# Kernel optimization log

Hardware: AMD Instinct MI355X
Metric: run time of the kernel (lower is better)

The kernel has to match this reference:

```python
import jax, jax.numpy as jnp
import numpy as np

N = 10000   # nodes
E = 100000  # edges (before self-loops)
H = 4       # heads (layers 0-3); last layer uses 1 head
C = 200     # out_channels per head
IN_DIMS = [200, H * C, H * C, H * C, H * C]
HEADS   = [H, H, H, H, 1]
NEG_SLOPE = 0.2  # PyG GATConv default


def _gat_layer(x, src, dst, W, a_src, a_dst, b, heads):
    # x: [N, Fin], W: [Fin, heads*C], a_src/a_dst: [heads, C], b: [heads*C]
    h = (x @ W).reshape(N, heads, C)                       # [N,H,C]
    alpha_src = jnp.einsum('nhc,hc->nh', h, a_src)         # [N,H]
    alpha_dst = jnp.einsum('nhc,hc->nh', h, a_dst)         # [N,H]
    e = jax.nn.leaky_relu(alpha_src[src] + alpha_dst[dst], NEG_SLOPE)  # [E',H]
    # segment softmax over incoming edges of each dst node
    m = jax.ops.segment_max(e, dst, num_segments=N)        # [N,H]
    ex = jnp.exp(e - m[dst])                               # [E',H]
    den = jax.ops.segment_sum(ex, dst, num_segments=N)     # [N,H]
    alpha = ex / den[dst]                                  # [E',H]
    out = jax.ops.segment_sum(h[src] * alpha[:, :, None], dst, num_segments=N)
    return out.reshape(N, heads * C) + b, alpha


def setup_inputs() -> dict:
    key = jax.random.key(0)
    ks = jax.random.split(key, 2 + 4 * 5)
    inp = {}
    inp['X'] = jax.random.normal(ks[0], (N, 200), jnp.float32)
    inp['edge_index'] = jax.random.randint(ks[1], (2, E), 0, N, dtype=jnp.int32)
    k = 2
    for i in range(5):
        fin, hd = IN_DIMS[i], HEADS[i]
        s = 1.0 / np.sqrt(fin)
        inp[f'W{i}'] = jax.random.normal(ks[k], (fin, hd * C), jnp.float32) * s; k += 1
        inp[f'as{i}'] = jax.random.normal(ks[k], (hd, C), jnp.float32) * s; k += 1
        inp[f'ad{i}'] = jax.random.normal(ks[k], (hd, C), jnp.float32) * s; k += 1
        inp[f'b{i}'] = jnp.zeros((hd * C,), jnp.float32); k += 1
    return inp


def reference(X, edge_index,
              W0, as0, ad0, b0, W1, as1, ad1, b1, W2, as2, ad2, b2,
              W3, as3, ad3, b3, W4, as4, ad4, b4):
    # add self-loops (PyG GATConv default add_self_loops=True)
    loops = jnp.arange(N, dtype=edge_index.dtype)
    src = jnp.concatenate([edge_index[0], loops])
    dst = jnp.concatenate([edge_index[1], loops])
    gelu = lambda v: jax.nn.gelu(v, approximate=False)
    # eval mode: all dropouts are identity
    x, _ = _gat_layer(X, src, dst, W0, as0, ad0, b0, HEADS[0]); x = gelu(x)
    x, _ = _gat_layer(x, src, dst, W1, as1, ad1, b1, HEADS[1]); x = gelu(x)
    x, _ = _gat_layer(x, src, dst, W2, as2, ad2, b2, HEADS[2]); x = gelu(x)
    x, _ = _gat_layer(x, src, dst, W3, as3, ad3, b3, HEADS[3]); x = gelu(x)
    x, edge_attn = _gat_layer(x, src, dst, W4, as4, ad4, b4, HEADS[4])
    x = gelu(x)
    return (x, edge_attn)
```

## Files before the change

### kernel.cpp

```cpp
#include <hip/hip_runtime.h>
#include <math.h>

#define NN 10000
#define EE 100000
#define EPE 110000
#define CC 200
#define MPAD 10112

typedef __attribute__((ext_vector_type(8))) _Float16 f16x8;
typedef __attribute__((ext_vector_type(4))) _Float16 f16x4;
typedef __attribute__((ext_vector_type(4))) unsigned short u16x4;
typedef __attribute__((ext_vector_type(4))) float f32x4;

__device__ __forceinline__ float lrelu(float v) { return v >= 0.f ? v : 0.2f * v; }
__device__ __forceinline__ float gelu_f(float v) { return 0.5f * v * (1.f + erff(v * 0.70710678118654752f)); }


__global__ void build_edges_kernel(const int* __restrict__ ei,
                                   int* __restrict__ src_all, int* __restrict__ dst_all,
                                   int* __restrict__ deg) {
    int e = blockIdx.x * blockDim.x + threadIdx.x;
    if (e >= EPE) return;
    int s, d;
    if (e < EE) { s = ei[e]; d = ei[EE + e]; }
    else        { s = e - EE; d = e - EE; }
    src_all[e] = s;
    dst_all[e] = d;
    atomicAdd(&deg[d], 1);
}

__global__ void scan_kernel(const int* __restrict__ deg, int* __restrict__ row_ptr, int n) {
    __shared__ int wsum[16];
    int tid = threadIdx.x;
    int lane = tid & 63, w = tid >> 6;
    int carry = 0;
    for (int base = 0; base < n; base += 1024) {
        int idx = base + tid;
        int v = (idx < n) ? deg[idx] : 0;
        int x = v;
#pragma unroll
        for (int off = 1; off < 64; off <<= 1) {
            int t = __shfl_up(x, off);
            if (lane >= off) x += t;
        }
        if (lane == 63) wsum[w] = x;
        __syncthreads();
        if (w == 0) {
            int s = (lane < 16) ? wsum[lane] : 0;
#pragma unroll
            for (int off = 1; off < 16; off <<= 1) {
                int t = __shfl_up(s, off);
                if (lane >= off) s += t;
            }
            if (lane < 16) wsum[lane] = s;
        }
        __syncthreads();
        int woff = (w > 0) ? wsum[w - 1] : 0;
        if (idx < n) row_ptr[idx] = carry + woff + x - v;
        carry += wsum[15];
        __syncthreads();
    }
    if (tid == 0) row_ptr[n] = carry;
}

__global__ void scatter_kernel(const int* __restrict__ src_all, const int* __restrict__ dst_all,
                               const int* __restrict__ row_ptr, int* __restrict__ cursor,
                               int* __restrict__ col_src, int* __restrict__ col_eid) {
    int e = blockIdx.x * blockDim.x + threadIdx.x;
    if (e >= EPE) return;
    int d = dst_all[e];
    int pos = row_ptr[d] + atomicAdd(&cursor[d], 1);
    col_src[pos] = src_all[e];
    col_eid[pos] = e;
}


__global__ void convA_kernel(const float* __restrict__ x, int sx, int Fin, int Kp,
                             unsigned short* __restrict__ Ap) {
    size_t idx = (size_t)blockIdx.x * 256 + threadIdx.x;
    if (idx >= (size_t)MPAD * Kp) return;
    int row = (int)(idx / Kp);
    int kk  = (int)(idx % Kp);
    float v = 0.f;
    if (row < NN && kk < Fin) v = x[(size_t)row * sx + kk];
    Ap[idx] = __builtin_bit_cast(unsigned short, (_Float16)v);
}

__global__ void padA_kernel(unsigned short* __restrict__ Ap) {
    int idx = blockIdx.x * 256 + threadIdx.x;
    if (idx < NN * 32) {
        int rw = idx >> 5, c = idx & 31;
        Ap[(size_t)rw * 832 + 800 + c] = 0;
    } else {
        int j = idx - NN * 32;
        if (j < (MPAD - NN) * 832) {
            int rw = j / 832, c = j - rw * 832;
            Ap[(size_t)(NN + rw) * 832 + c] = 0;
        }
    }
}

__global__ void convB_kernel(const float* __restrict__ W, int Fin, int HC, int Kp, int Np,
                             unsigned short* __restrict__ Bp) {
    size_t idx = (size_t)blockIdx.x * 256 + threadIdx.x;
    if (idx >= (size_t)Np * Kp) return;
    int n  = (int)(idx / Kp);
    int kk = (int)(idx % Kp);
    float v = 0.f;
    if (n < HC && kk < Fin) v = W[(size_t)kk * HC + n];
    Bp[idx] = __builtin_bit_cast(unsigned short, (_Float16)v);
}


__global__ __launch_bounds__(256) void gemm_mfma(const unsigned short* __restrict__ A,
                                                 const unsigned short* __restrict__ B,
                                                 unsigned short* __restrict__ C,
                                                 int Kt, int Np, int ncol) {
    __shared__ unsigned short As[2][4096];
    __shared__ unsigned short Bs[2][8192];

    int tid = threadIdx.x;
    int lane = tid & 63, wave = tid >> 6;

    int nwg = gridDim.x;
    int orig = blockIdx.x;
    int q = nwg >> 3, r = nwg & 7;
    int xcd = orig & 7, sidx = orig >> 3;
    int wg = (xcd < r ? xcd * (q + 1) : r * (q + 1) + (xcd - r) * q) + sidx;
    int rowT = wg / ncol, colT = wg - rowT * ncol;
    int row0 = rowT * 64, col0 = colT * 128;
    int wr = wave >> 1, wc = wave & 1;

    size_t gAoff[2], gBoff[4];
    int ldsSegA[2], ldsSegB[4];
#pragma unroll
    for (int i = 0; i < 2; ++i) {
        int seg = wave * 2 + i;
        int chunkIdx = seg * 64 + lane;
        int rr = chunkIdx >> 3;
        int c = chunkIdx & 7;
        int cg = c ^ (rr & 7);
        gAoff[i] = (size_t)(row0 + rr) * Kt + (size_t)cg * 8;
        ldsSegA[i] = seg * 512;
    }
#pragma unroll
    for (int i = 0; i < 4; ++i) {
        int seg = wave * 4 + i;
        int chunkIdx = seg * 64 + lane;
        int rr = chunkIdx >> 3;
        int c = chunkIdx & 7;
        int cg = c ^ (rr & 7);
        gBoff[i] = (size_t)(col0 + rr) * Kt + (size_t)cg * 8;
        ldsSegB[i] = seg * 512;
    }

    int rowA[2], rowB[4];
#pragma unroll
    for (int m = 0; m < 2; ++m) rowA[m] = wr * 32 + m * 16 + (lane & 15);
#pragma unroll
    for (int n = 0; n < 4; ++n) rowB[n] = wc * 64 + n * 16 + (lane & 15);

    f32x4 acc[2][4];
#pragma unroll
    for (int m = 0; m < 2; ++m)
#pragma unroll
        for (int n = 0; n < 4; ++n) acc[m][n] = f32x4{0.f, 0.f, 0.f, 0.f};

#define STAGE(bufi, kk)                                                                     \
    _Pragma("unroll")                                                                       \
    for (int i = 0; i < 2; ++i)                                                             \
        __builtin_amdgcn_global_load_lds(                                                   \
            (const __attribute__((address_space(1))) void*)(A + gAoff[i] + (kk)),           \
            (__attribute__((address_space(3))) void*)(&As[bufi][ldsSegA[i]]), 16, 0, 0);    \
    _Pragma("unroll")                                                                       \
    for (int i = 0; i < 4; ++i)                                                             \
        __builtin_amdgcn_global_load_lds(                                                   \
            (const __attribute__((address_space(1))) void*)(B + gBoff[i] + (kk)),           \
            (__attribute__((address_space(3))) void*)(&Bs[bufi][ldsSegB[i]]), 16, 0, 0);

    int nk = Kt >> 6;
    STAGE(0, 0)

    for (int t = 0; t < nk; ++t) {
        int cur = t & 1;
        if (t + 1 < nk) {
            STAGE(1 - cur, (t + 1) * 64)
            asm volatile("s_waitcnt vmcnt(6)" ::: "memory");
        } else {
            asm volatile("s_waitcnt vmcnt(0)" ::: "memory");
        }
        __builtin_amdgcn_s_barrier();
        __builtin_amdgcn_sched_barrier(0);

        const unsigned short* asb = As[cur];
        const unsigned short* bsb = Bs[cur];
#pragma unroll
        for (int kh = 0; kh < 2; ++kh) {
            int cw = kh * 4 + (lane >> 4);
            f16x8 a[2], b[4];
#pragma unroll
            for (int m = 0; m < 2; ++m) {
                int ia = rowA[m] * 64 + ((cw ^ (rowA[m] & 7)) << 3);
                a[m] = *(const f16x8*)(&asb[ia]);
            }
#pragma unroll
            for (int n = 0; n < 4; ++n) {
                int ib = rowB[n] * 64 + ((cw ^ (rowB[n] & 7)) << 3);
                b[n] = *(const f16x8*)(&bsb[ib]);
            }
            if (kh == 0) __builtin_amdgcn_s_setprio(1);
#pragma unroll
            for (int m = 0; m < 2; ++m)
#pragma unroll
                for (int n = 0; n < 4; ++n)
                    acc[m][n] = __builtin_amdgcn_mfma_f32_16x16x32_f16(a[m], b[n], acc[m][n], 0, 0, 0);
        }
        __builtin_amdgcn_s_setprio(0);
        asm volatile("s_waitcnt lgkmcnt(0)" ::: "memory");
        __builtin_amdgcn_sched_barrier(0);
        __builtin_amdgcn_s_barrier();
        __builtin_amdgcn_sched_barrier(0);
    }
#undef STAGE

    int crow = row0 + wr * 32 + ((lane >> 4) << 2);
    int ccol = col0 + wc * 64 + (lane & 15);
#pragma unroll
    for (int m = 0; m < 2; ++m)
#pragma unroll
        for (int j = 0; j < 4; ++j) {
            size_t rb = (size_t)(crow + m * 16 + j) * Np;
#pragma unroll
            for (int n = 0; n < 4; ++n)
                C[rb + ccol + n * 16] =
                    __builtin_bit_cast(unsigned short, (_Float16)acc[m][n][j]);
        }
}


__global__ void attn_kernel(const unsigned short* __restrict__ h,
                            const float* __restrict__ a_s, const float* __restrict__ a_d,
                            float* __restrict__ asrc, float* __restrict__ adst,
                            int H, int HCp) {
    int n = blockIdx.x;
    int wave = threadIdx.x >> 6;
    int lane = threadIdx.x & 63;
    if (wave >= H) return;
    float sa = 0.f, da = 0.f;
    int c0 = lane * 4;
    if (c0 < CC) {
        f16x4 hv = *(const f16x4*)(h + (size_t)n * HCp + wave * CC + c0);
        float4 av = *(const float4*)(a_s + wave * CC + c0);
        float4 dv = *(const float4*)(a_d + wave * CC + c0);
        float h0 = (float)hv[0], h1 = (float)hv[1], h2 = (float)hv[2], h3 = (float)hv[3];
        sa = h0 * av.x + h1 * av.y + h2 * av.z + h3 * av.w;
        da = h0 * dv.x + h1 * dv.y + h2 * dv.z + h3 * dv.w;
    }
#pragma unroll
    for (int off = 32; off > 0; off >>= 1) {
        sa += __shfl_down(sa, off);
        da += __shfl_down(da, off);
    }
    if (lane == 0) {
        asrc[n * H + wave] = sa;
        adst[n * H + wave] = da;
    }
}


__global__ void mden_weight_kernel(const float* __restrict__ asrc, const float* __restrict__ adst,
                                   const int* __restrict__ row_ptr, const int* __restrict__ col_src,
                                   const int* __restrict__ col_eid,
                                   float* __restrict__ w, int H) {
    int i = blockIdx.x * blockDim.x + threadIdx.x;
    if (i >= NN * H) return;
    int n = i / H, hd = i - n * H;
    float ad = adst[i];
    int beg = row_ptr[n], end = row_ptr[n + 1];
    float m = -1e30f, den = 0.f;
    for (int e = beg; e < end; ++e) {
        int s = col_src[e];
        float v = lrelu(asrc[s * H + hd] + ad);
        if (v > m) { den = den * expf(m - v) + 1.f; m = v; }
        else den += expf(v - m);
    }
    float inv = 1.f / den;
    for (int e = beg; e < end; ++e) {
        int s = col_src[e];
        float v = lrelu(asrc[s * H + hd] + ad);
        w[(size_t)col_eid[e] * H + hd] = expf(v - m) * inv;
    }
}


__global__ __launch_bounds__(256) void agg3_kernel(const unsigned short* __restrict__ h,
                                                   const float* __restrict__ w,
                                                   const int* __restrict__ row_ptr,
                                                   const int* __restrict__ col_src,
                                                   const int* __restrict__ col_eid,
                                                   const float* __restrict__ bias,
                                                   float* __restrict__ out32,
                                                   unsigned short* __restrict__ apn,
                                                   int H, int HC, int HCp) {
    int n = blockIdx.x;
    int hc0 = threadIdx.x * 4;
    if (hc0 >= HC) return;
    int head = hc0 / CC;
    int beg = row_ptr[n], end = row_ptr[n + 1];

    float a0 = 0.f, a1 = 0.f, a2 = 0.f, a3 = 0.f;
    int s = col_src[beg], eid = col_eid[beg];
    float wv = w[(size_t)eid * H + head];
    f16x4 hv = *(const f16x4*)(h + (size_t)s * HCp + hc0);
    for (int e = beg; e < end; ++e) {
        int s2 = 0, eid2 = 0; float wv2 = 0.f; f16x4 hv2 = {};
        if (e + 1 < end) {
            s2 = col_src[e + 1]; eid2 = col_eid[e + 1];
            wv2 = w[(size_t)eid2 * H + head];
            hv2 = *(const f16x4*)(h + (size_t)s2 * HCp + hc0);
        }
        a0 += wv * (float)hv[0];
        a1 += wv * (float)hv[1];
        a2 += wv * (float)hv[2];
        a3 += wv * (float)hv[3];
        s = s2; eid = eid2; wv = wv2; hv = hv2;
    }
    float4 bv = *(const float4*)(bias + hc0);
    float g0 = gelu_f(a0 + bv.x), g1 = gelu_f(a1 + bv.y);
    float g2 = gelu_f(a2 + bv.z), g3 = gelu_f(a3 + bv.w);
    if (out32) {
        *(float4*)(out32 + (size_t)n * HC + hc0) = float4{g0, g1, g2, g3};
    } else {
        *(u16x4*)(apn + (size_t)n * 832 + hc0) = u16x4{
            __builtin_bit_cast(unsigned short, (_Float16)g0),
            __builtin_bit_cast(unsigned short, (_Float16)g1),
            __builtin_bit_cast(unsigned short, (_Float16)g2),
            __builtin_bit_cast(unsigned short, (_Float16)g3)};
    }
}


extern "C" void kernel_launch(void* const* d_in, const int* in_sizes, int n_in,
                              void* d_out, int out_size, void* d_ws, size_t ws_size,
                              hipStream_t stream) {
    const float* X = (const float*)d_in[0];
    const int* ei = (const int*)d_in[1];

    char* ws = (char*)d_ws;
    size_t off = 0;
    auto alloc = [&](size_t bytes) { void* p = ws + off; off += (bytes + 255) & ~(size_t)255; return p; };

    unsigned short* Ap0 = (unsigned short*)alloc((size_t)MPAD * 256 * 2);
    unsigned short* Ap  = (unsigned short*)alloc((size_t)MPAD * 832 * 2);
    unsigned short* Bp  = (unsigned short*)alloc((size_t)896 * 832 * 2);
    unsigned short* hbuf= (unsigned short*)alloc((size_t)MPAD * 896 * 2);
    float* asrc   = (float*)alloc((size_t)NN * 4 * 4);
    float* adst   = (float*)alloc((size_t)NN * 4 * 4);
    float* wbuf   = (float*)alloc((size_t)EPE * 4 * 4);
    int* src_all  = (int*)alloc((size_t)EPE * 4);
    int* dst_all  = (int*)alloc((size_t)EPE * 4);
    int* col_src  = (int*)alloc((size_t)EPE * 4);
    int* col_eid  = (int*)alloc((size_t)EPE * 4);
    int* row_ptr  = (int*)alloc((size_t)(NN + 1) * 4);
    int* degcur   = (int*)alloc((size_t)2 * NN * 4);
    int* deg = degcur, * cursor = degcur + NN;

    hipMemsetAsync(degcur, 0, 2 * NN * sizeof(int), stream);

    int eb = (EPE + 255) / 256;
    build_edges_kernel<<<eb, 256, 0, stream>>>(ei, src_all, dst_all, deg);
    scan_kernel<<<1, 1024, 0, stream>>>(deg, row_ptr, NN);
    scatter_kernel<<<eb, 256, 0, stream>>>(src_all, dst_all, row_ptr, cursor, col_src, col_eid);

    {
        int npad = NN * 32 + (MPAD - NN) * 832;
        padA_kernel<<<(npad + 255) / 256, 256, 0, stream>>>(Ap);
    }
    {
        size_t na = (size_t)MPAD * 256;
        convA_kernel<<<(int)((na + 255) / 256), 256, 0, stream>>>(X, 200, 200, 256, Ap0);
    }

    for (int i = 0; i < 5; ++i) {
        int Fin = (i == 0) ? 200 : 800;
        int H   = (i == 4) ? 1 : 4;
        int HC  = H * CC;
        int Kp  = (Fin == 200) ? 256 : 832;
        int Np  = (HC == 800) ? 896 : 256;
        int ncol = Np / 128;
        const unsigned short* Acur = (i == 0) ? Ap0 : Ap;
        const float* W   = (const float*)d_in[2 + 4 * i];
        const float* as_ = (const float*)d_in[3 + 4 * i];
        const float* ad_ = (const float*)d_in[4 + 4 * i];
        const float* b_  = (const float*)d_in[5 + 4 * i];

        size_t nb = (size_t)Np * Kp;
        convB_kernel<<<(int)((nb + 255) / 256), 256, 0, stream>>>(W, Fin, HC, Kp, Np, Bp);

        gemm_mfma<<<ncol * (MPAD / 64), 256, 0, stream>>>(Acur, Bp, hbuf, Kp, Np, ncol);

        attn_kernel<<<NN, 256, 0, stream>>>(hbuf, as_, ad_, asrc, adst, H, Np);

        float* wptr = (i == 4) ? (float*)d_out + (size_t)NN * CC : wbuf;
        mden_weight_kernel<<<(NN * H + 255) / 256, 256, 0, stream>>>(asrc, adst, row_ptr,
                                                                     col_src, col_eid, wptr, H);

        float* out32 = (i == 4) ? (float*)d_out : nullptr;
        unsigned short* apn = (i == 4) ? nullptr : Ap;
        agg3_kernel<<<NN, 256, 0, stream>>>(hbuf, wptr, row_ptr, col_src, col_eid, b_,
                                            out32, apn, H, HC, Np);
    }
}
```

Baseline: 543.2 us.

## Fuse attention logits into GEMM epilogue and softmax into aggregation kernel

Computes the per-node source/destination attention scores inside the GEMM epilogue by reducing over each tile's accumulators and atomically adding the partial sums, which removes the separate attention kernel and its re-read of h. The segment softmax (max/denominator) moves into the aggregation kernel as a wave-parallel reduction, and edge weights are recomputed on the fly in LDS, so weights are written to global memory only for the final layer. Weight conversion for all five layers is batched into one launch. The atomics add contention and make the scores depend on summation order, and the aggregation kernel gains block-level syncs per 64-edge chunk.

```diff
diff --git a/kernel.cpp b/kernel.cpp
--- a/kernel.cpp
+++ b/kernel.cpp
@@ -100,22 +100,33 @@
     }
 }
 
-__global__ void convB_kernel(const float* __restrict__ W, int Fin, int HC, int Kp, int Np,
-                             unsigned short* __restrict__ Bp) {
-    size_t idx = (size_t)blockIdx.x * 256 + threadIdx.x;
-    if (idx >= (size_t)Np * Kp) return;
-    int n  = (int)(idx / Kp);
-    int kk = (int)(idx % Kp);
+__global__ void convB_all_kernel(const float* __restrict__ W0, const float* __restrict__ W1,
+                                 const float* __restrict__ W2, const float* __restrict__ W3,
+                                 const float* __restrict__ W4,
+                                 unsigned short* __restrict__ Bp) {
+    int l = blockIdx.y;
+    const float* W = (l == 0) ? W0 : (l == 1) ? W1 : (l == 2) ? W2 : (l == 3) ? W3 : W4;
+    int Fin = (l == 0) ? 200 : 800;
+    int HC  = (l == 4) ? 200 : 800;
+    int Kp  = (l == 0) ? 256 : 832;
+    int Np  = (l == 4) ? 256 : 896;
+    int idx = blockIdx.x * 256 + threadIdx.x;
+    if (idx >= Np * Kp) return;
+    int n = idx / Kp, kk = idx - n * Kp;
     float v = 0.f;
     if (n < HC && kk < Fin) v = W[(size_t)kk * HC + n];
-    Bp[idx] = __builtin_bit_cast(unsigned short, (_Float16)v);
+    Bp[(size_t)l * (896 * 832) + idx] = __builtin_bit_cast(unsigned short, (_Float16)v);
 }
 
 
 __global__ __launch_bounds__(256) void gemm_mfma(const unsigned short* __restrict__ A,
                                                  const unsigned short* __restrict__ B,
                                                  unsigned short* __restrict__ C,
-                                                 int Kt, int Np, int ncol) {
+                                                 const float* __restrict__ a_s,
+                                                 const float* __restrict__ a_d,
+                                                 float* __restrict__ g_asrc,
+                                                 float* __restrict__ g_adst,
+                                                 int Kt, int Np, int ncol, int HC, int H) {
     __shared__ unsigned short As[2][4096];
     __shared__ unsigned short Bs[2][8192];
 
@@ -235,107 +246,152 @@
                 C[rb + ccol + n * 16] =
                     __builtin_bit_cast(unsigned short, (_Float16)acc[m][n][j]);
         }
-}
-
-
-__global__ void attn_kernel(const unsigned short* __restrict__ h,
-                            const float* __restrict__ a_s, const float* __restrict__ a_d,
-                            float* __restrict__ asrc, float* __restrict__ adst,
-                            int H, int HCp) {
+
+    int base = col0 + wc * 64;
+    int hA = base / CC;
+    float sAs[2][8], sAd[2][8];
+#pragma unroll
+    for (int b = 0; b < 2; ++b)
+#pragma unroll
+        for (int k = 0; k < 8; ++k) { sAs[b][k] = 0.f; sAd[b][k] = 0.f; }
+#pragma unroll
+    for (int n = 0; n < 4; ++n) {
+        int c = ccol + n * 16;
+        if (c < HC) {
+            int hd = c / CC;
+            int cm = c - hd * CC;
+            float asv = a_s[hd * CC + cm];
+            float adv = a_d[hd * CC + cm];
+            int b = hd - hA;
+#pragma unroll
+            for (int m = 0; m < 2; ++m)
+#pragma unroll
+                for (int j = 0; j < 4; ++j) {
+                    sAs[b][m * 4 + j] += acc[m][n][j] * asv;
+                    sAd[b][m * 4 + j] += acc[m][n][j] * adv;
+                }
+        }
+    }
+#pragma unroll
+    for (int off = 1; off < 16; off <<= 1) {
+#pragma unroll
+        for (int b = 0; b < 2; ++b)
+#pragma unroll
+            for (int k = 0; k < 8; ++k) {
+                sAs[b][k] += __shfl_xor(sAs[b][k], off);
+                sAd[b][k] += __shfl_xor(sAd[b][k], off);
+            }
+    }
+    if ((lane & 15) == 0) {
+#pragma unroll
+        for (int b = 0; b < 2; ++b) {
+            int hd = hA + b;
+            if (hd >= H) continue;
+#pragma unroll
+            for (int m = 0; m < 2; ++m)
+#pragma unroll
+                for (int j = 0; j < 4; ++j) {
+                    int row = crow + m * 16 + j;
+                    if (row < NN) {
+                        atomicAdd(&g_asrc[row * H + hd], sAs[b][m * 4 + j]);
+                        atomicAdd(&g_adst[row * H + hd], sAd[b][m * 4 + j]);
+                    }
+                }
+        }
+    }
+}
+
+
+__global__ __launch_bounds__(256) void fused_agg_kernel(const unsigned short* __restrict__ h,
+                                                        const float* __restrict__ asrc,
+                                                        const float* __restrict__ adst,
+                                                        const int* __restrict__ row_ptr,
+                                                        const int* __restrict__ col_src,
+                                                        const int* __restrict__ col_eid,
+                                                        const float* __restrict__ bias,
+                                                        float* __restrict__ out32,
+                                                        unsigned short* __restrict__ apn,
+                                                        float* __restrict__ wout,
+                                                        int H, int HC, int HCp) {
     int n = blockIdx.x;
-    int wave = threadIdx.x >> 6;
-    int lane = threadIdx.x & 63;
-    if (wave >= H) return;
-    float sa = 0.f, da = 0.f;
-    int c0 = lane * 4;
-    if (c0 < CC) {
-        f16x4 hv = *(const f16x4*)(h + (size_t)n * HCp + wave * CC + c0);
-        float4 av = *(const float4*)(a_s + wave * CC + c0);
-        float4 dv = *(const float4*)(a_d + wave * CC + c0);
-        float h0 = (float)hv[0], h1 = (float)hv[1], h2 = (float)hv[2], h3 = (float)hv[3];
-        sa = h0 * av.x + h1 * av.y + h2 * av.z + h3 * av.w;
-        da = h0 * dv.x + h1 * dv.y + h2 * dv.z + h3 * dv.w;
-    }
-#pragma unroll
-    for (int off = 32; off > 0; off >>= 1) {
-        sa += __shfl_down(sa, off);
-        da += __shfl_down(da, off);
-    }
-    if (lane == 0) {
-        asrc[n * H + wave] = sa;
-        adst[n * H + wave] = da;
-    }
-}
-
-
-__global__ void mden_weight_kernel(const float* __restrict__ asrc, const float* __restrict__ adst,
-                                   const int* __restrict__ row_ptr, const int* __restrict__ col_src,
-                                   const int* __restrict__ col_eid,
-                                   float* __restrict__ w, int H) {
-    int i = blockIdx.x * blockDim.x + threadIdx.x;
-    if (i >= NN * H) return;
-    int n = i / H, hd = i - n * H;
-    float ad = adst[i];
+    int tid = threadIdx.x;
+    int wave = tid >> 6, lane = tid & 63;
     int beg = row_ptr[n], end = row_ptr[n + 1];
-    float m = -1e30f, den = 0.f;
-    for (int e = beg; e < end; ++e) {
-        int s = col_src[e];
-        float v = lrelu(asrc[s * H + hd] + ad);
-        if (v > m) { den = den * expf(m - v) + 1.f; m = v; }
-        else den += expf(v - m);
-    }
-    float inv = 1.f / den;
-    for (int e = beg; e < end; ++e) {
-        int s = col_src[e];
-        float v = lrelu(asrc[s * H + hd] + ad);
-        w[(size_t)col_eid[e] * H + hd] = expf(v - m) * inv;
-    }
-}
-
-
-__global__ __launch_bounds__(256) void agg3_kernel(const unsigned short* __restrict__ h,
-                                                   const float* __restrict__ w,
-                                                   const int* __restrict__ row_ptr,
-                                                   const int* __restrict__ col_src,
-                                                   const int* __restrict__ col_eid,
-                                                   const float* __restrict__ bias,
-                                                   float* __restrict__ out32,
-                                                   unsigned short* __restrict__ apn,
-                                                   int H, int HC, int HCp) {
-    int n = blockIdx.x;
-    int hc0 = threadIdx.x * 4;
-    if (hc0 >= HC) return;
-    int head = hc0 / CC;
-    int beg = row_ptr[n], end = row_ptr[n + 1];
-
+
+    __shared__ float m_s[4], inv_s[4], ad_s[4];
+    __shared__ float w_lds[64 * 4];
+    __shared__ int src_lds[64];
+
+    if (wave < H) {
+        float ad = adst[n * H + wave];
+        float m = -1e30f, den = 0.f;
+        for (int e = beg + lane; e < end; e += 64) {
+            float v = lrelu(asrc[col_src[e] * H + wave] + ad);
+            if (v > m) { den = den * expf(m - v) + 1.f; m = v; }
+            else den += expf(v - m);
+        }
+#pragma unroll
+        for (int off = 1; off < 64; off <<= 1) {
+            float m2 = __shfl_xor(m, off);
+            float d2 = __shfl_xor(den, off);
+            float M = fmaxf(m, m2);
+            den = den * expf(m - M) + d2 * expf(m2 - M);
+            m = M;
+        }
+        if (lane == 0) { m_s[wave] = m; inv_s[wave] = 1.f / den; ad_s[wave] = ad; }
+    }
+    __syncthreads();
+
+    int ch0 = tid * 4;
+    int head = ch0 / CC;
     float a0 = 0.f, a1 = 0.f, a2 = 0.f, a3 = 0.f;
-    int s = col_src[beg], eid = col_eid[beg];
-    float wv = w[(size_t)eid * H + head];
-    f16x4 hv = *(const f16x4*)(h + (size_t)s * HCp + hc0);
-    for (int e = beg; e < end; ++e) {
-        int s2 = 0, eid2 = 0; float wv2 = 0.f; f16x4 hv2 = {};
-        if (e + 1 < end) {
-            s2 = col_src[e + 1]; eid2 = col_eid[e + 1];
-            wv2 = w[(size_t)eid2 * H + head];
-            hv2 = *(const f16x4*)(h + (size_t)s2 * HCp + hc0);
-        }
-        a0 += wv * (float)hv[0];
-        a1 += wv * (float)hv[1];
-        a2 += wv * (float)hv[2];
-        a3 += wv * (float)hv[3];
-        s = s2; eid = eid2; wv = wv2; hv = hv2;
-    }
-    float4 bv = *(const float4*)(bias + hc0);
-    float g0 = gelu_f(a0 + bv.x), g1 = gelu_f(a1 + bv.y);
-    float g2 = gelu_f(a2 + bv.z), g3 = gelu_f(a3 + bv.w);
-    if (out32) {
-        *(float4*)(out32 + (size_t)n * HC + hc0) = float4{g0, g1, g2, g3};
-    } else {
-        *(u16x4*)(apn + (size_t)n * 832 + hc0) = u16x4{
-            __builtin_bit_cast(unsigned short, (_Float16)g0),
-            __builtin_bit_cast(unsigned short, (_Float16)g1),
-            __builtin_bit_cast(unsigned short, (_Float16)g2),
-            __builtin_bit_cast(unsigned short, (_Float16)g3)};
+
+    for (int c0 = beg; c0 < end; c0 += 64) {
+        int cnt = min(64, end - c0);
+        if (wave < H && lane < cnt) {
+            int e = c0 + lane;
+            int s = col_src[e];
+            float v = lrelu(asrc[s * H + wave] + ad_s[wave]);
+            float wv = expf(v - m_s[wave]) * inv_s[wave];
+            w_lds[lane * 4 + wave] = wv;
+            if (wave == 0) src_lds[lane] = s;
+            if (wout) wout[(size_t)col_eid[e] * H + wave] = wv;
+        }
+        __syncthreads();
+        if (ch0 < HC) {
+            int s = src_lds[0];
+            float wv = w_lds[head];
+            f16x4 hv = *(const f16x4*)(h + (size_t)s * HCp + ch0);
+            for (int j = 0; j < cnt; ++j) {
+                float wv2 = 0.f; f16x4 hv2 = {};
+                if (j + 1 < cnt) {
+                    int s2 = src_lds[j + 1];
+                    wv2 = w_lds[(j + 1) * 4 + head];
+                    hv2 = *(const f16x4*)(h + (size_t)s2 * HCp + ch0);
+                }
+                a0 += wv * (float)hv[0];
+                a1 += wv * (float)hv[1];
+                a2 += wv * (float)hv[2];
+                a3 += wv * (float)hv[3];
+                wv = wv2; hv = hv2;
+            }
+        }
+        __syncthreads();
+    }
+
+    if (ch0 < HC) {
+        float4 bv = *(const float4*)(bias + ch0);
+        float g0 = gelu_f(a0 + bv.x), g1 = gelu_f(a1 + bv.y);
+        float g2 = gelu_f(a2 + bv.z), g3 = gelu_f(a3 + bv.w);
+        if (out32) {
+            *(float4*)(out32 + (size_t)n * HC + ch0) = float4{g0, g1, g2, g3};
+        } else {
+            *(u16x4*)(apn + (size_t)n * 832 + ch0) = u16x4{
+                __builtin_bit_cast(unsigned short, (_Float16)g0),
+                __builtin_bit_cast(unsigned short, (_Float16)g1),
+                __builtin_bit_cast(unsigned short, (_Float16)g2),
+                __builtin_bit_cast(unsigned short, (_Float16)g3)};
+        }
     }
 }
 
@@ -352,11 +408,9 @@
 
     unsigned short* Ap0 = (unsigned short*)alloc((size_t)MPAD * 256 * 2);
     unsigned short* Ap  = (unsigned short*)alloc((size_t)MPAD * 832 * 2);
-    unsigned short* Bp  = (unsigned short*)alloc((size_t)896 * 832 * 2);
+    unsigned short* Bp  = (unsigned short*)alloc((size_t)5 * 896 * 832 * 2);
     unsigned short* hbuf= (unsigned short*)alloc((size_t)MPAD * 896 * 2);
-    float* asrc   = (float*)alloc((size_t)NN * 4 * 4);
-    float* adst   = (float*)alloc((size_t)NN * 4 * 4);
-    float* wbuf   = (float*)alloc((size_t)EPE * 4 * 4);
+    float* attn_all = (float*)alloc((size_t)5 * 2 * NN * 4 * 4);
     int* src_all  = (int*)alloc((size_t)EPE * 4);
     int* dst_all  = (int*)alloc((size_t)EPE * 4);
     int* col_src  = (int*)alloc((size_t)EPE * 4);
@@ -366,6 +420,7 @@
     int* deg = degcur, * cursor = degcur + NN;
 
     hipMemsetAsync(degcur, 0, 2 * NN * sizeof(int), stream);
+    hipMemsetAsync(attn_all, 0, (size_t)5 * 2 * NN * 4 * 4, stream);
 
     int eb = (EPE + 255) / 256;
     build_edges_kernel<<<eb, 256, 0, stream>>>(ei, src_all, dst_all, deg);
@@ -380,34 +435,31 @@
         size_t na = (size_t)MPAD * 256;
         convA_kernel<<<(int)((na + 255) / 256), 256, 0, stream>>>(X, 200, 200, 256, Ap0);
     }
+    convB_all_kernel<<<dim3((896 * 832 + 255) / 256, 5), 256, 0, stream>>>(
+        (const float*)d_in[2], (const float*)d_in[6], (const float*)d_in[10],
+        (const float*)d_in[14], (const float*)d_in[18], Bp);
 
     for (int i = 0; i < 5; ++i) {
-        int Fin = (i == 0) ? 200 : 800;
         int H   = (i == 4) ? 1 : 4;
         int HC  = H * CC;
-        int Kp  = (Fin == 200) ? 256 : 832;
-        int Np  = (HC == 800) ? 896 : 256;
+        int Kp  = (i == 0) ? 256 : 832;
+        int Np  = (i == 4) ? 256 : 896;
         int ncol = Np / 128;
         const unsigned short* Acur = (i == 0) ? Ap0 : Ap;
-        const float* W   = (const float*)d_in[2 + 4 * i];
+        const unsigned short* Bpl = Bp + (size_t)i * (896 * 832);
         const float* as_ = (const float*)d_in[3 + 4 * i];
         const float* ad_ = (const float*)d_in[4 + 4 * i];
         const float* b_  = (const float*)d_in[5 + 4 * i];
-
-        size_t nb = (size_t)Np * Kp;
-        convB_kernel<<<(int)((nb + 255) / 256), 256, 0, stream>>>(W, Fin, HC, Kp, Np, Bp);
-
-        gemm_mfma<<<ncol * (MPAD / 64), 256, 0, stream>>>(Acur, Bp, hbuf, Kp, Np, ncol);
-
-        attn_kernel<<<NN, 256, 0, stream>>>(hbuf, as_, ad_, asrc, adst, H, Np);
-
-        float* wptr = (i == 4) ? (float*)d_out + (size_t)NN * CC : wbuf;
-        mden_weight_kernel<<<(NN * H + 255) / 256, 256, 0, stream>>>(asrc, adst, row_ptr,
-                                                                     col_src, col_eid, wptr, H);
+        float* asrc_l = attn_all + (size_t)i * 2 * NN * 4;
+        float* adst_l = asrc_l + NN * 4;
+
+        gemm_mfma<<<ncol * (MPAD / 64), 256, 0, stream>>>(Acur, Bpl, hbuf, as_, ad_,
+                                                          asrc_l, adst_l, Kp, Np, ncol, HC, H);
 
         float* out32 = (i == 4) ? (float*)d_out : nullptr;
         unsigned short* apn = (i == 4) ? nullptr : Ap;
-        agg3_kernel<<<NN, 256, 0, stream>>>(hbuf, wptr, row_ptr, col_src, col_eid, b_,
-                                            out32, apn, H, HC, Np);
-    }
-}
+        float* wout = (i == 4) ? (float*)d_out + (size_t)NN * CC : nullptr;
+        fused_agg_kernel<<<NN, 256, 0, stream>>>(hbuf, asrc_l, adst_l, row_ptr, col_src,
+                                                 col_eid, b_, out32, apn, wout, H, HC, Np);
+    }
+}
```

Result: slower. 597.1 us (+9.9%).
